# Optimization experiments

Hardware: AMD Instinct MI355X
Metric: run time of the kernel (lower is better)

Reference implementation:

```python
import jax, jax.numpy as jnp
import numpy as np

B, L, D_MODEL = 8, 256, 256
D_STATE, D_INNER, DT_RANK, D_CONV = 16, 512, 16, 4


def _ln(x, g, b, eps):
    mu = x.mean(-1, keepdims=True)
    var = ((x - mu) ** 2).mean(-1, keepdims=True)
    return (x - mu) * jax.lax.rsqrt(var + eps) * g + b


def _ssm(x, W_in, conv_w, conv_b, W_x, W_dt, b_dt, A_log, Dp, W_out):
    # x: (B, L, D_MODEL) -- standard Mamba selective-scan block
    xz = x @ W_in                                  # (B,L,2*Di)
    xc, z = jnp.split(xz, 2, axis=-1)
    K = conv_w.shape[-1]
    xp = jnp.pad(xc, ((0, 0), (K - 1, 0), (0, 0)))  # causal depthwise conv
    xc = sum(xp[:, k:k + L, :] * conv_w[:, k] for k in range(K)) + conv_b
    xc = jax.nn.silu(xc)
    x_dbl = xc @ W_x                               # (B,L,R+2S)
    dt, Bm, Cm = jnp.split(x_dbl, [DT_RANK, DT_RANK + D_STATE], axis=-1)
    dt = jax.nn.softplus(dt @ W_dt + b_dt)         # (B,L,Di)
    A = -jnp.exp(A_log)                            # (Di,S)
    dA = jnp.exp(dt[..., None] * A)                # (B,L,Di,S)
    dBx = dt[..., None] * Bm[:, :, None, :] * xc[..., None]

    def step(h, inp):
        dA_t, dBx_t, C_t = inp
        h = dA_t * h + dBx_t                       # (B,Di,S)
        y = jnp.einsum('bds,bs->bd', h, C_t)
        return h, y

    h0 = jnp.zeros((xc.shape[0], D_INNER, D_STATE), xc.dtype)
    xs = (dA.transpose(1, 0, 2, 3), dBx.transpose(1, 0, 2, 3), Cm.transpose(1, 0, 2))
    _, ys = jax.lax.scan(step, h0, xs)             # (L,B,Di)
    y = ys.transpose(1, 0, 2) + xc * Dp
    y = y * jax.nn.silu(z)
    return y @ W_out


def _basic(x, ln_g, ln_b, ssm_params):
    # Basic_Block: ReLU(SSM(LN(x))) + x  (drop_path=0, attn_drop=0)
    return jax.nn.relu(_ssm(_ln(x, ln_g, ln_b, 1e-6), *ssm_params)) + x


def setup_inputs() -> dict:
    key = jax.random.key(0)
    ks = jax.random.split(key, 32)

    def n(k, shape, s=0.02):
        return jax.random.normal(k, shape, dtype=jnp.float32) * s

    inp = {}
    inp['x_spa'] = jax.random.normal(ks[0], (B, L, D_MODEL), dtype=jnp.float32)
    inp['x_spe'] = jax.random.normal(ks[1], (B, L, D_MODEL), dtype=jnp.float32)
    i = 2
    A_init = jnp.log(jnp.tile(jnp.arange(1, D_STATE + 1, dtype=jnp.float32), (D_INNER, 1)))
    for p in ('spa', 'spe'):
        inp[p + '_ln_g'] = jnp.ones((D_MODEL,), jnp.float32)
        inp[p + '_ln_b'] = jnp.zeros((D_MODEL,), jnp.float32)
        inp[p + '_W_in'] = n(ks[i], (D_MODEL, 2 * D_INNER)); i += 1
        inp[p + '_conv_w'] = n(ks[i], (D_INNER, D_CONV), 0.1); i += 1
        inp[p + '_conv_b'] = jnp.zeros((D_INNER,), jnp.float32)
        inp[p + '_W_x'] = n(ks[i], (D_INNER, DT_RANK + 2 * D_STATE)); i += 1
        inp[p + '_W_dt'] = n(ks[i], (DT_RANK, D_INNER), 0.1); i += 1
        inp[p + '_b_dt'] = n(ks[i], (D_INNER,), 0.1); i += 1
        inp[p + '_A_log'] = A_init
        inp[p + '_D'] = jnp.ones((D_INNER,), jnp.float32)
        inp[p + '_W_out'] = n(ks[i], (D_INNER, D_MODEL)); i += 1
    inp['sc_W'] = n(ks[i], (D_MODEL, D_MODEL)); i += 1
    inp['sc_b'] = jnp.zeros((D_MODEL,), jnp.float32)
    inp['sc_ln_g'] = jnp.ones((D_MODEL,), jnp.float32)
    inp['sc_ln_b'] = jnp.zeros((D_MODEL,), jnp.float32)
    inp['fusion_W'] = n(ks[i], (D_MODEL, D_MODEL))
    return inp


def reference(x_spa, x_spe,
              spa_ln_g, spa_ln_b, spa_W_in, spa_conv_w, spa_conv_b, spa_W_x,
              spa_W_dt, spa_b_dt, spa_A_log, spa_D, spa_W_out,
              spe_ln_g, spe_ln_b, spe_W_in, spe_conv_w, spe_conv_b, spe_W_x,
              spe_W_dt, spe_b_dt, spe_A_log, spe_D, spe_W_out,
              sc_W, sc_b, sc_ln_g, sc_ln_b, fusion_W):
    # shared shortcut: Linear + LayerNorm (eps=1e-5)
    ident_spa = _ln(x_spa @ sc_W + sc_b, sc_ln_g, sc_ln_b, 1e-5)
    ident_spe = _ln(x_spe @ sc_W + sc_b, sc_ln_g, sc_ln_b, 1e-5)
    spa_p = (spa_W_in, spa_conv_w, spa_conv_b, spa_W_x, spa_W_dt, spa_b_dt, spa_A_log, spa_D, spa_W_out)
    spe_p = (spe_W_in, spe_conv_w, spe_conv_b, spe_W_x, spe_W_dt, spe_b_dt, spe_A_log, spe_D, spe_W_out)
    a = _basic(x_spa, spa_ln_g, spa_ln_b, spa_p)
    e = _basic(x_spe, spe_ln_g, spe_ln_b, spe_p)
    # fusion gate: mean-pool both branches, Linear(no bias) + sigmoid, broadcast-mul
    fw = jax.nn.sigmoid(((a.mean(1) + e.mean(1)) * 0.5) @ fusion_W)[:, None, :]
    a = a * fw
    e = e * fw
    return (a + ident_spa, e + ident_spe)
```

## Files before the change

kernel.cpp:

```cpp
#include <hip/hip_runtime.h>
#include <hip/hip_bf16.h>
#include <math.h>

#define BD 8
#define LD 256
#define DM 256
#define DS 16
#define DI 512
#define RK 16

#define NROWS (2*BD*LD)
#define HALF_ROWS (BD*LD)

typedef __attribute__((ext_vector_type(8))) short bhalf8;
typedef __attribute__((ext_vector_type(4))) float f32x4;

__device__ __forceinline__ float siluf(float x){ return x / (1.f + __expf(-x)); }
__device__ __forceinline__ float softplusf(float x){
  return fmaxf(x, 0.f) + log1pf(__expf(-fabsf(x)));
}
__device__ __forceinline__ unsigned short f2bf(float f){
  __hip_bfloat16 h = __float2bfloat16(f);
  return *reinterpret_cast<unsigned short*>(&h);
}


__global__ __launch_bounds__(256) void k_prep(
    const float* __restrict__ Wi_spa, const float* __restrict__ Wi_spe,
    const float* __restrict__ Wo_spa, const float* __restrict__ Wo_spe,
    const float* __restrict__ scW,
    const float* __restrict__ Wx_spa, const float* __restrict__ Wx_spe,
    const float* __restrict__ x_spa, const float* __restrict__ x_spe,
    const float* __restrict__ g_spa, const float* __restrict__ b_spa,
    const float* __restrict__ g_spe, const float* __restrict__ b_spe,
    unsigned short* __restrict__ Wt_i_spa, unsigned short* __restrict__ Wt_i_spe,
    unsigned short* __restrict__ Wt_o_spa, unsigned short* __restrict__ Wt_o_spe,
    unsigned short* __restrict__ scWt,
    unsigned short* __restrict__ Wxt_spa, unsigned short* __restrict__ Wxt_spe,
    unsigned short* __restrict__ xnbf, unsigned short* __restrict__ xbf,
    float* __restrict__ pooled)
{
  __shared__ __align__(16) unsigned char smem[59904];
  int b = blockIdx.x;
  int tid = threadIdx.x;
  if (b == 60){
    for (int i=tid; i<BD*DM; i+=256) pooled[i] = 0.f;
    return;
  }
  if (b >= 61){
    float (*xst)[260] = (float (*)[260])smem;
    float (*red)[16]  = (float (*)[16])(smem + 16640);
    float *mu = (float*)(smem + 17664);
    float *rs = (float*)(smem + 17728);
    int r0g = (b - 61) * 16;
    int branch = r0g >= HALF_ROWS;
    const float* xb = branch ? x_spe : x_spa;
    const float* g  = branch ? g_spe : g_spa;
    const float* be = branch ? b_spe : b_spa;
    int rr0 = branch ? r0g - HALF_ROWS : r0g;
    for (int p=0;p<4;p++){
      int i4 = tid + 256*p;
      int r = i4 >> 6, c4 = (i4 & 63)*4;
      *(float4*)&xst[r][c4] = *(const float4*)(xb + (rr0+r)*DM + c4);
    }
    __syncthreads();
    {
      int row = tid >> 4, seg = tid & 15;
      float s = 0.f, s2 = 0.f;
      #pragma unroll
      for (int i=0;i<4;i++){
        float4 v = *(float4*)&xst[row][seg*16 + i*4];
        s  += v.x+v.y+v.z+v.w;
        s2 += v.x*v.x + v.y*v.y + v.z*v.z + v.w*v.w;
      }
      red[row][seg] = s;
      __syncthreads();
      if (seg == 0){
        float t=0.f;
        #pragma unroll
        for (int i=0;i<16;i++) t += red[row][i];
        mu[row] = t * (1.f/DM);
      }
      __syncthreads();
      red[row][seg] = s2;
      __syncthreads();
      if (seg == 0){
        float t=0.f;
        #pragma unroll
        for (int i=0;i<16;i++) t += red[row][i];
        float m = mu[row];
        rs[row] = rsqrtf(t*(1.f/DM) - m*m + 1e-6f);
      }
    }
    __syncthreads();
    for (int p=0;p<4;p++){
      int i4 = tid + 256*p;
      int r = i4 >> 6, c4 = (i4 & 63)*4;
      float4 v  = *(float4*)&xst[r][c4];
      float4 gv = *(const float4*)(g + c4);
      float4 bv = *(const float4*)(be + c4);
      float m = mu[r], rv = rs[r];
      unsigned int rlo = (unsigned int)f2bf(v.x) | ((unsigned int)f2bf(v.y) << 16);
      unsigned int rhi = (unsigned int)f2bf(v.z) | ((unsigned int)f2bf(v.w) << 16);
      *(uint2*)&xbf[(r0g+r)*DM + c4] = make_uint2(rlo, rhi);
      unsigned int nlo = (unsigned int)f2bf((v.x-m)*rv*gv.x + bv.x)
                       | ((unsigned int)f2bf((v.y-m)*rv*gv.y + bv.y) << 16);
      unsigned int nhi = (unsigned int)f2bf((v.z-m)*rv*gv.z + bv.z)
                       | ((unsigned int)f2bf((v.w-m)*rv*gv.w + bv.w) << 16);
      *(uint2*)&xnbf[(r0g+r)*DM + c4] = make_uint2(nlo, nhi);
    }
    return;
  }
  if (b >= 52){
    int bb = b - 52;
    int branch = bb >> 2, chunk = bb & 3;
    int k0 = chunk*128;
    const float* Wx = branch ? Wx_spe : Wx_spa;
    unsigned short* Wxt = branch ? Wxt_spe : Wxt_spa;
    float (*tile2)[49] = (float (*)[49])(smem + 34816);
    for (int i=tid; i<128*48; i+=256){
      int kk = i/48, c = i - kk*48;
      tile2[kk][c] = Wx[(k0+kk)*48 + c];
    }
    __syncthreads();
    for (int i=tid; i<64*128; i+=256){
      int cc = i >> 7, kk = i & 127;
      float v = (cc < 48) ? tile2[kk][cc] : 0.f;
      int kg = k0 + kk;
      int ct = cc >> 4, m16 = cc & 15;
      int ks = kg >> 5, quad = (kg >> 3) & 3, j = kg & 7;
      Wxt[((ct*16 + ks)*64 + quad*16 + m16)*8 + j] = f2bf(v);
    }
    return;
  }
  unsigned short (*tile)[68] = (unsigned short (*)[68])smem;
  const float* W; unsigned short* Wt; int N, K, c0, k0;
  if (b < 32){
    int bb = b & 15;
    W  = (b < 16) ? Wi_spa  : Wi_spe;
    Wt = (b < 16) ? Wt_i_spa: Wt_i_spe;
    N = 1024; K = 256; c0 = (bb >> 2)*256; k0 = (bb & 3)*64;
  } else if (b < 48){
    int bb = b - 32; int h = bb >> 3; bb &= 7;
    W  = h ? Wo_spe  : Wo_spa;
    Wt = h ? Wt_o_spe: Wt_o_spa;
    N = 256; K = 512; c0 = 0; k0 = bb*64;
  } else {
    int bb = b - 48;
    W = scW; Wt = scWt;
    N = 256; K = 256; c0 = 0; k0 = bb*64;
  }
  int c = c0 + tid;
  #pragma unroll 8
  for (int kk=0; kk<64; kk++)
    tile[tid][kk] = f2bf(W[(k0+kk)*N + c]);
  __syncthreads();
  int ksegs = K >> 5;
  for (int p=0; p<16; p++){
    int i = tid + 256*p;
    int cl = i >> 4, kq = (i & 15)*4;
    int cg = c0 + cl;
    int ct = cg >> 4, m16 = cg & 15;
    int kg = k0 + kq;
    int ks = kg >> 5, quad = (kg >> 3) & 3, j = kg & 7;
    uint2 v = *(const uint2*)&tile[cl][kq];
    *(uint2*)&Wt[((ct*ksegs + ks)*64 + quad*16 + m16)*8 + j] = v;
  }
}

__global__ __launch_bounds__(256) void k_gemm1(
    const unsigned short* __restrict__ xnbf, const unsigned short* __restrict__ xbf,
    const unsigned short* __restrict__ Wt_spa, const unsigned short* __restrict__ Wt_spe,
    const unsigned short* __restrict__ scWt, const float* __restrict__ sc_b,
    const float* __restrict__ ln_g, const float* __restrict__ ln_b,
    float* __restrict__ xc_raw, float* __restrict__ szout, float* __restrict__ ident)
{
  __shared__ unsigned short At[16][264];
  __shared__ float Dt[16][260];
  __shared__ float red[16][16];
  __shared__ float mu[16], rs[16];
  int tid = threadIdx.x;
  int bi = blockIdx.x;
  int w = tid >> 6, lane = tid & 63;
  int m16 = lane & 15, quad = lane >> 4;
  if (bi < 1024){
    int rg = bi >> 2, cg = bi & 3;
    int r0 = rg * 16;
    int branch = (r0 >= HALF_ROWS);
    const unsigned short* Wt = branch ? Wt_spe : Wt_spa;
    for (int p=0;p<2;p++){
      int i = tid + 256*p;
      int r = i >> 5, oct = (i & 31)*8;
      *(uint4*)&At[r][oct] = *(const uint4*)&xnbf[(r0+r)*DM + oct];
    }
    __syncthreads();
    bhalf8 af[8];
    #pragma unroll
    for (int ks=0; ks<8; ks++)
      af[ks] = *(const bhalf8*)&At[m16][ks*32 + quad*8];
    f32x4 acc[4];
    #pragma unroll
    for (int ct=0; ct<4; ct++) acc[ct] = (f32x4)(0.f);
    #pragma unroll
    for (int ks=0; ks<8; ks++){
      #pragma unroll
      for (int ct=0; ct<4; ct++){
        int f = (cg*16 + w*4 + ct)*8 + ks;
        bhalf8 bf = *(const bhalf8*)&Wt[f*512 + lane*8];
        acc[ct] = __builtin_amdgcn_mfma_f32_16x16x32_bf16(af[ks], bf, acc[ct], 0,0,0);
      }
    }
    bool isz = (cg >= 2);
    float* outp = isz ? szout : xc_raw;
    int cbase = (cg & 1)*256 + w*64;
    #pragma unroll
    for (int ct=0; ct<4; ct++){
      #pragma unroll
      for (int e=0;e<4;e++){
        int row = r0 + quad*4 + e;
        int col = cbase + ct*16 + m16;
        float v = acc[ct][e];
        if (isz) v = siluf(v);
        outp[row*DI + col] = v;
      }
    }
  } else {
    int r0 = (bi - 1024) * 16;
    for (int p=0;p<2;p++){
      int i = tid + 256*p;
      int r = i >> 5, oct = (i & 31)*8;
      *(uint4*)&At[r][oct] = *(const uint4*)&xbf[(r0+r)*DM + oct];
    }
    __syncthreads();
    bhalf8 af[8];
    #pragma unroll
    for (int ks=0; ks<8; ks++)
      af[ks] = *(const bhalf8*)&At[m16][ks*32 + quad*8];
    f32x4 acc[4];
    #pragma unroll
    for (int ct=0; ct<4; ct++) acc[ct] = (f32x4)(0.f);
    #pragma unroll
    for (int ks=0; ks<8; ks++){
      #pragma unroll
      for (int ct=0; ct<4; ct++){
        int f = (w*4 + ct)*8 + ks;
        bhalf8 bf = *(const bhalf8*)&scWt[f*512 + lane*8];
        acc[ct] = __builtin_amdgcn_mfma_f32_16x16x32_bf16(af[ks], bf, acc[ct], 0,0,0);
      }
    }
    #pragma unroll
    for (int ct=0; ct<4; ct++){
      #pragma unroll
      for (int e=0;e<4;e++){
        int row = quad*4 + e;
        int col = w*64 + ct*16 + m16;
        Dt[row][col] = acc[ct][e] + sc_b[col];
      }
    }
    __syncthreads();
    {
      int row = tid >> 4, seg = tid & 15;
      float s = 0.f, s2 = 0.f;
      #pragma unroll
      for (int i=0;i<4;i++){
        float4 v = *(const float4*)&Dt[row][seg*16 + i*4];
        s  += v.x+v.y+v.z+v.w;
        s2 += v.x*v.x + v.y*v.y + v.z*v.z + v.w*v.w;
      }
      red[row][seg] = s;
      __syncthreads();
      if (seg == 0){
        float t=0.f;
        #pragma unroll
        for (int i=0;i<16;i++) t += red[row][i];
        mu[row] = t * (1.f/DM);
      }
      __syncthreads();
      red[row][seg] = s2;
      __syncthreads();
      if (seg == 0){
        float t=0.f;
        #pragma unroll
        for (int i=0;i<16;i++) t += red[row][i];
        float m = mu[row];
        rs[row] = rsqrtf(t*(1.f/DM) - m*m + 1e-5f);
      }
    }
    __syncthreads();
    float gg = ln_g[tid], bb = ln_b[tid];
    #pragma unroll
    for (int r=0;r<16;r++)
      ident[(r0+r)*DM + tid] = (Dt[r][tid]-mu[r])*rs[r]*gg + bb;
  }
}

__global__ __launch_bounds__(256) void k_convdbl(
    const float* __restrict__ cw_spa, const float* __restrict__ cb_spa,
    const float* __restrict__ cw_spe, const float* __restrict__ cb_spe,
    const float* __restrict__ xc_raw,
    const unsigned short* __restrict__ Wxt_spa, const unsigned short* __restrict__ Wxt_spe,
    const float* __restrict__ Wdt_spa, const float* __restrict__ bdt_spa,
    const float* __restrict__ Wdt_spe, const float* __restrict__ bdt_spe,
    float* __restrict__ xc, float* __restrict__ dt,
    float* __restrict__ Bm, float* __restrict__ Cm)
{
  __shared__ unsigned short At[16][520];
  __shared__ float xdbl[16][18];
  int tid = threadIdx.x;
  int r0 = blockIdx.x * 16;
  int branch = r0 >= HALF_ROWS;
  int l0 = r0 & (LD-1);
  const float* cw = branch ? cw_spe : cw_spa;
  const float* cb = branch ? cb_spe : cb_spa;
  const unsigned short* Wxt = branch ? Wxt_spe : Wxt_spa;
  const float* Wdt = branch ? Wdt_spe : Wdt_spa;
  const float* bdt = branch ? bdt_spe : bdt_spa;
  {
    int c = tid*2;
    float4 w0 = *(const float4*)(cw + 4*c);
    float4 w1 = *(const float4*)(cw + 4*(c+1));
    float2 bias = *(const float2*)(cb + c);
    float2 h0, h1, h2;
    if (l0 > 0){
      h0 = *(const float2*)(xc_raw + (r0-3)*DI + c);
      h1 = *(const float2*)(xc_raw + (r0-2)*DI + c);
      h2 = *(const float2*)(xc_raw + (r0-1)*DI + c);
    } else {
      h0 = make_float2(0.f,0.f); h1 = h0; h2 = h0;
    }
    #pragma unroll
    for (int r=0;r<16;r++){
      float2 cur = *(const float2*)(xc_raw + (r0+r)*DI + c);
      float vx = bias.x;
      vx = fmaf(h0.x, w0.x, vx); vx = fmaf(h1.x, w0.y, vx);
      vx = fmaf(h2.x, w0.z, vx); vx = fmaf(cur.x, w0.w, vx);
      float vy = bias.y;
      vy = fmaf(h0.y, w1.x, vy); vy = fmaf(h1.y, w1.y, vy);
      vy = fmaf(h2.y, w1.z, vy); vy = fmaf(cur.y, w1.w, vy);
      vx = siluf(vx); vy = siluf(vy);
      *(float2*)(xc + (r0+r)*DI + c) = make_float2(vx, vy);
      unsigned int pk = (unsigned int)f2bf(vx) | ((unsigned int)f2bf(vy) << 16);
      *(unsigned int*)&At[r][c] = pk;
      h0 = h1; h1 = h2; h2 = cur;
    }
  }
  __syncthreads();
  int w = tid >> 6, lane = tid & 63;
  int m16 = lane & 15, quad = lane >> 4;
  f32x4 acc = (f32x4)(0.f);
  #pragma unroll
  for (int ks=0; ks<16; ks++){
    bhalf8 a = *(const bhalf8*)&At[m16][ks*32 + quad*8];
    int f = w*16 + ks;
    bhalf8 bf = *(const bhalf8*)&Wxt[f*512 + lane*8];
    acc = __builtin_amdgcn_mfma_f32_16x16x32_bf16(a, bf, acc, 0,0,0);
  }
  #pragma unroll
  for (int e=0;e<4;e++){
    int row = quad*4 + e;
    float v = acc[e];
    if (w == 0)      xdbl[row][m16] = v;
    else if (w == 1) Bm[(r0+row)*DS + m16] = v;
    else if (w == 2) Cm[(r0+row)*DS + m16] = v;
  }
  __syncthreads();
  float wdt0[16], wdt1[16];
  #pragma unroll
  for (int j=0;j<16;j++){ wdt0[j]=Wdt[j*DI+tid]; wdt1[j]=Wdt[j*DI+tid+256]; }
  float b0 = bdt[tid], b1 = bdt[tid+256];
  #pragma unroll
  for (int r=0;r<16;r++){
    float a0=b0, a1=b1;
    #pragma unroll
    for (int j=0;j<16;j++){
      float xv = xdbl[r][j];
      a0 = fmaf(xv, wdt0[j], a0);
      a1 = fmaf(xv, wdt1[j], a1);
    }
    dt[(r0+r)*DI + tid]       = softplusf(a0);
    dt[(r0+r)*DI + tid + 256] = softplusf(a1);
  }
}

__global__ __launch_bounds__(256) void k_scan(
    const float* __restrict__ Alog_spa, const float* __restrict__ Dp_spa,
    const float* __restrict__ Alog_spe, const float* __restrict__ Dp_spe,
    const float* __restrict__ dt, const float* __restrict__ xc,
    const float* __restrict__ sz, const float* __restrict__ Bm,
    const float* __restrict__ Cm, unsigned short* __restrict__ ybf)
{
  __shared__ float dts[32][20], xcs[32][20], szs[32][20], Bs[32][20], Cs[32][20];
  __shared__ float Dsh[16];
  int tid = threadIdx.x;
  int bi = blockIdx.x;
  int branch = bi >> 8;
  int rem = bi & 255;
  int b = rem >> 5;
  int d0 = (rem & 31) * 16;
  const float* Alog = branch ? Alog_spe : Alog_spa;
  const float* Dp   = branch ? Dp_spe   : Dp_spa;
  int dg = tid >> 4, s = tid & 15;
  int d = d0 + dg;
  float A_ds = -__expf(Alog[d*DS + s]);
  if (tid < 16) Dsh[tid] = Dp[d0 + tid];
  int row0 = branch*HALF_ROWS + b*LD;
  float h = 0.f;
  for (int c=0; c<8; c++){
    int rbase = row0 + c*32;
    for (int idx=tid; idx<640; idx+=256){
      int arr = idx >> 7;
      int j = idx & 127;
      int r = j >> 2, c4 = (j & 3)*4;
      float4 v;
      if      (arr == 0) v = *(const float4*)(dt + (rbase+r)*DI + d0 + c4);
      else if (arr == 1) v = *(const float4*)(xc + (rbase+r)*DI + d0 + c4);
      else if (arr == 2) v = *(const float4*)(sz + (rbase+r)*DI + d0 + c4);
      else if (arr == 3) v = *(const float4*)(Bm + (rbase+r)*DS + c4);
      else               v = *(const float4*)(Cm + (rbase+r)*DS + c4);
      if      (arr == 0) *(float4*)&dts[r][c4] = v;
      else if (arr == 1) *(float4*)&xcs[r][c4] = v;
      else if (arr == 2) *(float4*)&szs[r][c4] = v;
      else if (arr == 3) *(float4*)&Bs[r][c4]  = v;
      else               *(float4*)&Cs[r][c4]  = v;
    }
    __syncthreads();
    float yp[32];
    #pragma unroll
    for (int li=0; li<32; li++){
      float dtv = dts[li][dg];
      float xcv = xcs[li][dg];
      float dA = __expf(dtv * A_ds);
      h = fmaf(dA, h, dtv * Bs[li][s] * xcv);
      yp[li] = h * Cs[li][s];
    }
    #pragma unroll
    for (int li=0; li<32; li++){
      yp[li] += __shfl_xor(yp[li], 1, 64);
      yp[li] += __shfl_xor(yp[li], 2, 64);
      yp[li] += __shfl_xor(yp[li], 4, 64);
      yp[li] += __shfl_xor(yp[li], 8, 64);
    }
    {
      float Dv = Dsh[dg];
      float v0 = fmaf(xcs[s][dg],    Dv, yp[s])    * szs[s][dg];
      float v1 = fmaf(xcs[s+16][dg], Dv, yp[s+16]) * szs[s+16][dg];
      ybf[(rbase+s)*DI    + d0 + dg] = f2bf(v0);
      ybf[(rbase+s+16)*DI + d0 + dg] = f2bf(v1);
    }
    __syncthreads();
  }
}

__global__ __launch_bounds__(256) void k_wout(
    const unsigned short* __restrict__ Wt_spa, const unsigned short* __restrict__ Wt_spe,
    const float* __restrict__ x_spa, const float* __restrict__ x_spe,
    const unsigned short* __restrict__ ybf, float* __restrict__ ae,
    float* __restrict__ pooled)
{
  __shared__ unsigned short At[16][520];
  int tid = threadIdx.x;
  int bi = blockIdx.x;
  int r0 = (bi >> 1) * 16;
  int ch = bi & 1;
  int branch = (r0 >= HALF_ROWS);
  const unsigned short* Wt = branch ? Wt_spe : Wt_spa;
  const float* xb = branch ? x_spe : x_spa;
  int rr0 = branch ? r0 - HALF_ROWS : r0;
  for (int p=0;p<4;p++){
    int i = tid + 256*p;
    int r = i >> 6, oct = (i & 63)*8;
    *(uint4*)&At[r][oct] = *(const uint4*)&ybf[(r0+r)*DI + oct];
  }
  __syncthreads();
  int w = tid >> 6, lane = tid & 63;
  int m16 = lane & 15, quad = lane >> 4;
  bhalf8 af[16];
  #pragma unroll
  for (int ks=0; ks<16; ks++)
    af[ks] = *(const bhalf8*)&At[m16][ks*32 + quad*8];
  f32x4 acc[2];
  #pragma unroll
  for (int ct=0; ct<2; ct++) acc[ct] = (f32x4)(0.f);
  #pragma unroll
  for (int ks=0; ks<16; ks++){
    #pragma unroll
    for (int ct=0; ct<2; ct++){
      int f = (ch*8 + w*2 + ct)*16 + ks;
      bhalf8 bf = *(const bhalf8*)&Wt[f*512 + lane*8];
      acc[ct] = __builtin_amdgcn_mfma_f32_16x16x32_bf16(af[ks], bf, acc[ct], 0,0,0);
    }
  }
  float ps0 = 0.f, ps1 = 0.f;
  #pragma unroll
  for (int ct=0; ct<2; ct++){
    #pragma unroll
    for (int e=0;e<4;e++){
      int row = quad*4 + e;
      int col = ch*128 + w*32 + ct*16 + m16;
      float v = fmaxf(acc[ct][e], 0.f) + xb[(rr0+row)*DM + col];
      ae[(r0+row)*DM + col] = v;
      if (ct == 0) ps0 += v; else ps1 += v;
    }
  }
  ps0 += __shfl_xor(ps0, 16, 64); ps0 += __shfl_xor(ps0, 32, 64);
  ps1 += __shfl_xor(ps1, 16, 64); ps1 += __shfl_xor(ps1, 32, 64);
  if (quad == 0){
    int bidx = (r0 >> 8) & 7;
    atomicAdd(&pooled[bidx*DM + ch*128 + w*32 + m16],      ps0);
    atomicAdd(&pooled[bidx*DM + ch*128 + w*32 + 16 + m16], ps1);
  }
}

__global__ __launch_bounds__(256) void k_gate(const float* __restrict__ pooled,
    const float* __restrict__ fW, float* __restrict__ fw)
{
  __shared__ float p[DM];
  int b=blockIdx.x, c=threadIdx.x;
  p[c] = pooled[b*DM+c] * (0.5f/LD);
  __syncthreads();
  float a=0.f;
  for(int k=0;k<DM;k+=4){
    a = fmaf(p[k+0], fW[(k+0)*DM+c], a);
    a = fmaf(p[k+1], fW[(k+1)*DM+c], a);
    a = fmaf(p[k+2], fW[(k+2)*DM+c], a);
    a = fmaf(p[k+3], fW[(k+3)*DM+c], a);
  }
  fw[b*DM+c]=1.f/(1.f+__expf(-a));
}

__global__ __launch_bounds__(256) void k_final(const float* __restrict__ ae,
    const float* __restrict__ ident, const float* __restrict__ fw, float* __restrict__ out)
{
  int idx4 = blockIdx.x*256 + threadIdx.x;
  int row = idx4 >> 6;
  int b = (row >> 8) & 7;
  int c4 = (idx4 & 63) * 4;
  float4 av = *(const float4*)(ae + idx4*4);
  float4 iv = *(const float4*)(ident + idx4*4);
  float4 fv = *(const float4*)(fw + b*DM + c4);
  float4 o;
  o.x = fmaf(av.x, fv.x, iv.x);
  o.y = fmaf(av.y, fv.y, iv.y);
  o.z = fmaf(av.z, fv.z, iv.z);
  o.w = fmaf(av.w, fv.w, iv.w);
  *(float4*)(out + idx4*4) = o;
}

extern "C" void kernel_launch(void* const* d_in, const int* in_sizes, int n_in,
                              void* d_out, int out_size, void* d_ws, size_t ws_size,
                              hipStream_t stream) {
  const float* x_spa     = (const float*)d_in[0];
  const float* x_spe     = (const float*)d_in[1];
  const float* spa_ln_g  = (const float*)d_in[2];
  const float* spa_ln_b  = (const float*)d_in[3];
  const float* spa_W_in  = (const float*)d_in[4];
  const float* spa_cw    = (const float*)d_in[5];
  const float* spa_cb    = (const float*)d_in[6];
  const float* spa_W_x   = (const float*)d_in[7];
  const float* spa_W_dt  = (const float*)d_in[8];
  const float* spa_b_dt  = (const float*)d_in[9];
  const float* spa_A_log = (const float*)d_in[10];
  const float* spa_D     = (const float*)d_in[11];
  const float* spa_W_out = (const float*)d_in[12];
  const float* spe_ln_g  = (const float*)d_in[13];
  const float* spe_ln_b  = (const float*)d_in[14];
  const float* spe_W_in  = (const float*)d_in[15];
  const float* spe_cw    = (const float*)d_in[16];
  const float* spe_cb    = (const float*)d_in[17];
  const float* spe_W_x   = (const float*)d_in[18];
  const float* spe_W_dt  = (const float*)d_in[19];
  const float* spe_b_dt  = (const float*)d_in[20];
  const float* spe_A_log = (const float*)d_in[21];
  const float* spe_D     = (const float*)d_in[22];
  const float* spe_W_out = (const float*)d_in[23];
  const float* sc_W      = (const float*)d_in[24];
  const float* sc_b      = (const float*)d_in[25];
  const float* sc_ln_g   = (const float*)d_in[26];
  const float* sc_ln_b   = (const float*)d_in[27];
  const float* fusion_W  = (const float*)d_in[28];

  float* ws = (float*)d_ws;
  float* ident  = ws;
  float* xc_raw = ident  + NROWS*DM;
  float* sz     = xc_raw + NROWS*DI;
  float* xc     = sz     + NROWS*DI;
  float* dt     = xc     + NROWS*DI;
  float* Bm     = dt     + NROWS*DI;
  float* Cm     = Bm     + NROWS*DS;
  float* pooled = Cm     + NROWS*DS;
  float* fw     = pooled + BD*DM;
  unsigned short* Wt_i_spa = (unsigned short*)(fw + BD*DM);
  unsigned short* Wt_i_spe = Wt_i_spa + 1024*256;
  unsigned short* Wt_o_spa = Wt_i_spe + 1024*256;
  unsigned short* Wt_o_spe = Wt_o_spa + 256*512;
  unsigned short* scWt     = Wt_o_spe + 256*512;
  unsigned short* Wxt_spa  = scWt     + 256*256;
  unsigned short* Wxt_spe  = Wxt_spa  + 64*512;
  unsigned short* xnbf     = Wxt_spe  + 64*512;
  unsigned short* xbf      = xnbf     + NROWS*DM;

  float* out = (float*)d_out;

  k_prep<<<317, 256, 0, stream>>>(spa_W_in, spe_W_in, spa_W_out, spe_W_out, sc_W,
                                  spa_W_x, spe_W_x, x_spa, x_spe,
                                  spa_ln_g, spa_ln_b, spe_ln_g, spe_ln_b,
                                  Wt_i_spa, Wt_i_spe, Wt_o_spa, Wt_o_spe, scWt,
                                  Wxt_spa, Wxt_spe, xnbf, xbf, pooled);
  k_gemm1<<<1280, 256, 0, stream>>>(xnbf, xbf, Wt_i_spa, Wt_i_spe, scWt, sc_b,
                                    sc_ln_g, sc_ln_b, xc_raw, sz, ident);
  k_convdbl<<<NROWS/16, 256, 0, stream>>>(spa_cw, spa_cb, spe_cw, spe_cb, xc_raw,
                                          Wxt_spa, Wxt_spe,
                                          spa_W_dt, spa_b_dt, spe_W_dt, spe_b_dt,
                                          xc, dt, Bm, Cm);
  unsigned short* ybf = (unsigned short*)xc_raw;
  k_scan<<<512, 256, 0, stream>>>(spa_A_log, spa_D, spe_A_log, spe_D, dt, xc, sz, Bm, Cm, ybf);
  float* ae = dt;
  k_wout<<<512, 256, 0, stream>>>(Wt_o_spa, Wt_o_spe, x_spa, x_spe, ybf, ae, pooled);
  k_gate<<<BD, 256, 0, stream>>>(pooled, fusion_W, fw);
  k_final<<<NROWS*DM/1024, 256, 0, stream>>>(ae, ident, fw, out);
}
```

Baseline: 208.9 us.

## Load scan inputs directly into registers and reduce outputs via LDS transpose

The selective-scan kernel no longer stages dt/xc/sz/B/C chunks in shared memory. Each thread now reads its own 16-step inputs straight from global memory into registers, and the chunk length drops from 32 to 16. The 16-lane shuffle reduction over the state dimension is replaced by a skewed, double-buffered LDS write-then-sum, which needs only one barrier per chunk. This removes the staging copy, one barrier and many cross-lane shuffles, but adds redundant, poorly coalesced global loads (16 lanes share each dt/xc address) and dynamic register-array indexing for rxc[s].

Result: faster. 197.1 us (-5.7%).

```diff
diff --git a/kernel.cpp b/kernel.cpp
--- a/kernel.cpp
+++ b/kernel.cpp
@@ -389,7 +389,7 @@
     const float* __restrict__ sz, const float* __restrict__ Bm,
     const float* __restrict__ Cm, unsigned short* __restrict__ ybf)
 {
-  __shared__ float dts[32][20], xcs[32][20], szs[32][20], Bs[32][20], Cs[32][20];
+  __shared__ float ypbuf[2][16][257];
   __shared__ float Dsh[16];
   int tid = threadIdx.x;
   int bi = blockIdx.x;
@@ -404,50 +404,38 @@
   float A_ds = -__expf(Alog[d*DS + s]);
   if (tid < 16) Dsh[tid] = Dp[d0 + tid];
   int row0 = branch*HALF_ROWS + b*LD;
+  int wcol = s*16 + ((dg + s) & 15);
   float h = 0.f;
-  for (int c=0; c<8; c++){
-    int rbase = row0 + c*32;
-    for (int idx=tid; idx<640; idx+=256){
-      int arr = idx >> 7;
-      int j = idx & 127;
-      int r = j >> 2, c4 = (j & 3)*4;
-      float4 v;
-      if      (arr == 0) v = *(const float4*)(dt + (rbase+r)*DI + d0 + c4);
-      else if (arr == 1) v = *(const float4*)(xc + (rbase+r)*DI + d0 + c4);
-      else if (arr == 2) v = *(const float4*)(sz + (rbase+r)*DI + d0 + c4);
-      else if (arr == 3) v = *(const float4*)(Bm + (rbase+r)*DS + c4);
-      else               v = *(const float4*)(Cm + (rbase+r)*DS + c4);
-      if      (arr == 0) *(float4*)&dts[r][c4] = v;
-      else if (arr == 1) *(float4*)&xcs[r][c4] = v;
-      else if (arr == 2) *(float4*)&szs[r][c4] = v;
-      else if (arr == 3) *(float4*)&Bs[r][c4]  = v;
-      else               *(float4*)&Cs[r][c4]  = v;
-    }
-    __syncthreads();
-    float yp[32];
-    #pragma unroll
-    for (int li=0; li<32; li++){
-      float dtv = dts[li][dg];
-      float xcv = xcs[li][dg];
-      float dA = __expf(dtv * A_ds);
-      h = fmaf(dA, h, dtv * Bs[li][s] * xcv);
-      yp[li] = h * Cs[li][s];
-    }
-    #pragma unroll
-    for (int li=0; li<32; li++){
-      yp[li] += __shfl_xor(yp[li], 1, 64);
-      yp[li] += __shfl_xor(yp[li], 2, 64);
-      yp[li] += __shfl_xor(yp[li], 4, 64);
-      yp[li] += __shfl_xor(yp[li], 8, 64);
-    }
-    {
-      float Dv = Dsh[dg];
-      float v0 = fmaf(xcs[s][dg],    Dv, yp[s])    * szs[s][dg];
-      float v1 = fmaf(xcs[s+16][dg], Dv, yp[s+16]) * szs[s+16][dg];
-      ybf[(rbase+s)*DI    + d0 + dg] = f2bf(v0);
-      ybf[(rbase+s+16)*DI + d0 + dg] = f2bf(v1);
-    }
-    __syncthreads();
+  for (int c=0; c<16; c++){
+    int rbase = row0 + c*16;
+    int buf = c & 1;
+    float rdt[16], rxc[16], rB[16], rC[16];
+    #pragma unroll
+    for (int li=0; li<16; li++){
+      rdt[li] = dt[(rbase+li)*DI + d];
+      rxc[li] = xc[(rbase+li)*DI + d];
+      rB[li]  = Bm[(rbase+li)*DS + s];
+      rC[li]  = Cm[(rbase+li)*DS + s];
+    }
+    float yp[16];
+    #pragma unroll
+    for (int li=0; li<16; li++){
+      float dA = __expf(rdt[li] * A_ds);
+      h = fmaf(dA, h, rdt[li] * rB[li] * rxc[li]);
+      yp[li] = h * rC[li];
+    }
+    #pragma unroll
+    for (int li=0; li<16; li++)
+      ypbuf[buf][li][wcol] = yp[li];
+    __syncthreads();
+    float acc = 0.f;
+    #pragma unroll
+    for (int ss=0; ss<16; ss++)
+      acc += ypbuf[buf][s][ss*16 + ((dg + ss) & 15)];
+    float xcv = rxc[s];
+    float szv = sz[(rbase+s)*DI + d0 + dg];
+    float yv = fmaf(xcv, Dsh[dg], acc) * szv;
+    ybf[(rbase+s)*DI + d0 + dg] = f2bf(yv);
   }
 }
 
```
